# Optimization experiments

Hardware: AMD Instinct MI355X
Metric: run time of the kernel (lower is better)

## Reference

```python
import jax, jax.numpy as jnp
import numpy as np

B, S, E = 4, 2048, 768
H = 12
D = E // H  # 64

def setup_inputs() -> dict:
    key = jax.random.key(0)
    k_x, k_wqkv, k_wproj = jax.random.split(key, 3)
    x = jax.random.normal(k_x, (B, S, E), dtype=jnp.float32)
    w_qkv = jax.random.normal(k_wqkv, (E, 3 * E), dtype=jnp.float32) * 0.02
    b_qkv = jnp.zeros((3 * E,), dtype=jnp.float32)
    w_proj = jax.random.normal(k_wproj, (E, E), dtype=jnp.float32) * 0.02
    b_proj = jnp.zeros((E,), dtype=jnp.float32)
    return {"x": x, "w_qkv": w_qkv, "b_qkv": b_qkv, "w_proj": w_proj, "b_proj": b_proj}

def reference(x, w_qkv, b_qkv, w_proj, b_proj):
    # fused QKV projection: [B,S,E] -> [B,S,3E]
    qkv = jnp.einsum("bse,ef->bsf", x, w_qkv) + b_qkv
    qkv = qkv.reshape(B, S, 3, H, D)
    q, k, v = qkv[:, :, 0], qkv[:, :, 1], qkv[:, :, 2]  # [B,S,H,D]
    scale = 1.0 / jnp.sqrt(jnp.asarray(D, dtype=x.dtype))
    # causal scaled dot-product attention (explicit score matrix, as in module)
    scores = jnp.einsum("bshd,bthd->bhst", q, k) * scale  # [B,H,S,S]
    causal = jnp.tril(jnp.ones((S, S), dtype=bool))
    scores = jnp.where(causal, scores, jnp.finfo(scores.dtype).min)
    probs = jax.nn.softmax(scores, axis=-1)
    attn = jnp.einsum("bhst,bthd->bshd", probs, v).reshape(B, S, E)
    # output projection
    out = jnp.einsum("bse,ef->bsf", attn, w_proj) + b_proj
    return out
```

## Files before the change

### kernel.cpp

```cpp
#include <hip/hip_runtime.h>

#define SDIM 2048
#define EDIM 768
#define HDIM 12
#define DDIM 64
#define BDIM 4
#define MROWS (BDIM * SDIM)
#define NQKV (3 * EDIM)
#define NBH (BDIM * HDIM)
#define NTILE 32
#define NPAIR 16
#define NKT 24

typedef __attribute__((ext_vector_type(8))) short s16x8;
typedef __attribute__((ext_vector_type(4))) float f32x4;
typedef __attribute__((ext_vector_type(2))) unsigned int u32x2;

__device__ __forceinline__ short f2b(float x) {
  union { float f; unsigned u; } v; v.f = x;
  unsigned r = v.u + 0x7fffu + ((v.u >> 16) & 1u);
  return (short)(r >> 16);
}

__device__ __forceinline__ unsigned cvtpk(float lo, float hi) {
  unsigned r;
  asm volatile("v_cvt_pk_bf16_f32 %0, %1, %2" : "=v"(r) : "v"(lo), "v"(hi));
  return r;
}

__device__ __forceinline__ float fexp2(float x) {
  float r;
  asm("v_exp_f32 %0, %1" : "=v"(r) : "v"(x));
  return r;
}

__device__ __forceinline__ void gld16(const void* g, void* l) {
  __builtin_amdgcn_global_load_lds(
      (const __attribute__((address_space(1))) unsigned int*)g,
      (__attribute__((address_space(3))) unsigned int*)l, 16, 0, 0);
}

__global__ __launch_bounds__(256) void preproc(
    const float* __restrict__ x, const float* __restrict__ wqkv,
    const float* __restrict__ wproj, short* __restrict__ xb,
    short* __restrict__ wqkvt, short* __restrict__ wprojt) {
  const int bid = blockIdx.x;
  const int tid = threadIdx.x;
  const int l = tid & 63, w = tid >> 6;
  const int lr = l & 15, g = l >> 4;
  if (bid < 3072) {
    const int T = bid * 4 + w;
    const int rt = T / NKT, kt = T % NKT;
    const float* src = x + (size_t)(rt * 16 + lr) * EDIM + kt * 32 + g * 8;
    float4 v0 = *(const float4*)(src);
    float4 v1 = *(const float4*)(src + 4);
    s16x8 o;
    o[0] = f2b(v0.x); o[1] = f2b(v0.y); o[2] = f2b(v0.z); o[3] = f2b(v0.w);
    o[4] = f2b(v1.x); o[5] = f2b(v1.y); o[6] = f2b(v1.z); o[7] = f2b(v1.w);
    *(s16x8*)(xb + (size_t)T * 512 + l * 8) = o;
    return;
  }
  if (bid < 3072 + 864) {
    const int T = (bid - 3072) * 4 + w;
    const int ct = T / NKT, kt = T % NKT;
    s16x8 o;
#pragma unroll
    for (int j = 0; j < 8; ++j)
      o[j] = f2b(wqkv[(size_t)(kt * 32 + g * 8 + j) * NQKV + ct * 16 + lr]);
    *(s16x8*)(wqkvt + (size_t)T * 512 + l * 8) = o;
    return;
  }
  const int t = bid - 3072 - 864;
  const int n0 = (t % 24) * 32, k0 = (t / 24) * 32;
  __shared__ float tb[32][33];
  int tx = tid & 31, ty = tid >> 5;
#pragma unroll
  for (int i = 0; i < 4; ++i)
    tb[ty + 8 * i][tx] = wproj[(size_t)(k0 + ty + 8 * i) * EDIM + n0 + tx];
  __syncthreads();
#pragma unroll
  for (int i = 0; i < 4; ++i)
    wprojt[(size_t)(n0 + ty + 8 * i) * EDIM + k0 + tx] = f2b(tb[tx][ty + 8 * i]);
}

__global__ __launch_bounds__(256) void gemm_qkv(
    const short* __restrict__ A, const short* __restrict__ Bt,
    const float* __restrict__ bias, short* __restrict__ qout,
    short* __restrict__ kout, short* __restrict__ vout) {
  const int tid = threadIdx.x;
  const int l = tid & 63, w = tid >> 6;
  const int lr = l & 15, g = l >> 4;

  const int chunk = gridDim.x >> 3;
  const int sid = (blockIdx.x & 7) * chunk + (blockIdx.x >> 3);
  const int ntx = NQKV >> 7;
  const int bm = (sid / ntx) * 128, bn = (sid % ntx) * 128;
  const int wm = w >> 1, wn = w & 1;

  const short* Ab = A + ((size_t)(bm >> 4) + wm * 4) * NKT * 512 + l * 8;
  const short* Bb = Bt + ((size_t)(bn >> 4) + wn * 4) * NKT * 512 + l * 8;

  f32x4 acc[4][4];
  const f32x4 z4 = {0.f, 0.f, 0.f, 0.f};
#pragma unroll
  for (int m = 0; m < 4; ++m)
#pragma unroll
    for (int n = 0; n < 4; ++n) acc[m][n] = z4;

#pragma unroll 4
  for (int kt = 0; kt < NKT; ++kt) {
    s16x8 af[4], bf[4];
#pragma unroll
    for (int m = 0; m < 4; ++m)
      af[m] = *(const s16x8*)(Ab + (size_t)m * NKT * 512 + kt * 512);
#pragma unroll
    for (int n = 0; n < 4; ++n)
      bf[n] = *(const s16x8*)(Bb + (size_t)n * NKT * 512 + kt * 512);
    __builtin_amdgcn_s_setprio(1);
#pragma unroll
    for (int m = 0; m < 4; ++m)
#pragma unroll
      for (int n = 0; n < 4; ++n)
        acc[m][n] = __builtin_amdgcn_mfma_f32_16x16x32_bf16(af[m], bf[n],
                                                            acc[m][n], 0, 0, 0);
    __builtin_amdgcn_s_setprio(0);
  }

#pragma unroll
  for (int m = 0; m < 4; ++m) {
    int rbase = bm + wm * 64 + m * 16 + g * 4;
#pragma unroll
    for (int n = 0; n < 4; ++n) {
      int col = bn + wn * 64 + n * 16 + lr;
      float bv = bias[col];
      int which = (col >= 1536) ? 2 : (col >= 768 ? 1 : 0);
      int rem = col - which * 768;
      int h = rem >> 6, d = rem & 63;
#pragma unroll
      for (int i = 0; i < 4; ++i) {
        int r = rbase + i;
        int bb = r >> 11, s = r & 2047;
        short o = f2b(acc[m][n][i] + bv);
        size_t bh = (size_t)bb * HDIM + h;
        if (which == 0)      qout[(bh * SDIM + s) * DDIM + d] = o;
        else if (which == 1) kout[(bh * SDIM + s) * DDIM + d] = o;
        else                 vout[(bh * DDIM + d) * SDIM + s] = o;
      }
    }
  }
}

__global__ __launch_bounds__(256) void gemm_proj(
    const short* __restrict__ A, const short* __restrict__ Bt,
    const float* __restrict__ bias, int M, int N, int K,
    float* __restrict__ fout) {
  __shared__ char lds[3][16384];
  const int tid = threadIdx.x;
  const int l = tid & 63, w = tid >> 6;
  const int lr = l & 15, g = l >> 4;

  const int chunk = gridDim.x >> 3;
  const int sid = (blockIdx.x & 7) * chunk + (blockIdx.x >> 3);
  const int ntx = N >> 7;
  const int bm = (sid / ntx) * 128, bn = (sid % ntx) * 128;
  const int wm = w >> 1, wn = w & 1;

  const int srow = w * 32 + (l >> 2);
  const int sc8 = (((l & 3) ^ ((l >> 3) & 3)) << 3);
  const short* Ap0 = A + (size_t)(bm + srow) * K + sc8;
  const short* Bp0 = Bt + (size_t)(bn + srow) * K + sc8;

  f32x4 acc[4][4];
  const f32x4 z4 = {0.f, 0.f, 0.f, 0.f};
#pragma unroll
  for (int m = 0; m < 4; ++m)
#pragma unroll
    for (int n = 0; n < 4; ++n) acc[m][n] = z4;

#define STAGE(dst, t)                          \
  {                                            \
    char* Ad = (dst) + w * 2048;               \
    const short* Ap = Ap0 + (t) * 32;          \
    const short* Bp = Bp0 + (t) * 32;          \
    gld16(Ap, Ad);                             \
    gld16(Ap + 16 * K, Ad + 1024);             \
    gld16(Bp, Ad + 8192);                      \
    gld16(Bp + 16 * K, Ad + 9216);             \
  }

  const int nt = K >> 5;
  STAGE(lds[0], 0);
  STAGE(lds[1], 1);
  asm volatile("s_waitcnt vmcnt(4)" ::: "memory");
  __builtin_amdgcn_s_barrier();

  const int swz = ((lr >> 1) & 3) << 4;
  int bc = 0;
  for (int t = 0; t < nt; ++t) {
    if (t + 2 < nt) {
      int bs = bc + 2; if (bs >= 3) bs -= 3;
      STAGE(lds[bs], t + 2);
    }
    const char* Ab = lds[bc];
    const char* Bb = lds[bc] + 8192;
    s16x8 af[4], bfr[4];
#pragma unroll
    for (int m = 0; m < 4; ++m)
      af[m] = *(const s16x8*)(Ab + (wm * 64 + m * 16 + lr) * 64 + ((g << 4) ^ swz));
#pragma unroll
    for (int n = 0; n < 4; ++n)
      bfr[n] = *(const s16x8*)(Bb + (wn * 64 + n * 16 + lr) * 64 + ((g << 4) ^ swz));
    __builtin_amdgcn_s_setprio(1);
#pragma unroll
    for (int m = 0; m < 4; ++m)
#pragma unroll
      for (int n = 0; n < 4; ++n)
        acc[m][n] = __builtin_amdgcn_mfma_f32_16x16x32_bf16(af[m], bfr[n],
                                                            acc[m][n], 0, 0, 0);
    __builtin_amdgcn_s_setprio(0);
    if (t + 2 < nt) {
      asm volatile("s_waitcnt vmcnt(4)" ::: "memory");
      __builtin_amdgcn_s_barrier();
    } else if (t + 1 < nt) {
      asm volatile("s_waitcnt vmcnt(0)" ::: "memory");
      __builtin_amdgcn_s_barrier();
    }
    if (++bc == 3) bc = 0;
  }
#undef STAGE

#pragma unroll
  for (int m = 0; m < 4; ++m) {
    int rbase = bm + wm * 64 + m * 16 + g * 4;
#pragma unroll
    for (int n = 0; n < 4; ++n) {
      int col = bn + wn * 64 + n * 16 + lr;
      float bv = bias[col];
#pragma unroll
      for (int i = 0; i < 4; ++i)
        fout[(size_t)(rbase + i) * N + col] = acc[m][n][i] + bv;
    }
  }
}

__global__ __launch_bounds__(256, 3) void attn_mfma4(
    const short* __restrict__ qb, const short* __restrict__ kb,
    const short* __restrict__ vb, short* __restrict__ ao) {
  __shared__ short kvbuf[2][8192];
  __shared__ short pstrip[4][1024];

  const int tid = threadIdx.x;
  const int l = tid & 63, w = tid >> 6;
  const int lr = l & 15, g = l >> 4;
  const int swz = (lr & 7) << 4;

  const int lin = blockIdx.x;
  const int xcd = lin & 7;
  const int idx = lin >> 3;
  const int bh = xcd * 6 + (idx >> 4);
  const int pair = idx & 15;
  const int tiles[2] = {NTILE - 1 - pair, pair};

  const int b = bh / HDIM, h = bh % HDIM;
  const size_t base = (size_t)bh * SDIM * DDIM;

  const int srow = w * 16 + (l >> 3);
  const int sc = (l & 7) ^ (srow & 7);
  const size_t koff0 = (size_t)srow * DDIM + sc * 8;
  const size_t koff1 = (size_t)(srow + 8) * DDIM + sc * 8;
  const size_t voff0 = (size_t)srow * SDIM + sc * 8;
  const size_t voff1 = (size_t)(srow + 8) * SDIM + sc * 8;

  const float SC = 0.125f * 1.4426950408889634f;
  char* sw = (char*)pstrip[w];

#define KVSTAGE(buf_, kt_)                                        \
  {                                                               \
    char* kd = (char*)kvbuf[buf_] + w * 2048;                     \
    const short* kp = kb + base + (size_t)(kt_) * 64 * DDIM;      \
    const short* vp = vb + base + (size_t)(kt_) * 64;             \
    gld16(kp + koff0, kd);                                        \
    gld16(kp + koff1, kd + 1024);                                 \
    gld16(vp + voff0, kd + 8192);                                 \
    gld16(vp + voff1, kd + 9216);                                 \
  }

  for (int half = 0; half < 2; ++half) {
    const int tile = tiles[half];
    const int q0w = tile * 64 + w * 16;

    s16x8 qa[2];
#pragma unroll
    for (int s = 0; s < 2; ++s)
      qa[s] = *(const s16x8*)(qb + base + (size_t)(q0w + lr) * DDIM + s * 32 + g * 8);

    const f32x4 z4 = {0.f, 0.f, 0.f, 0.f};
    f32x4 acco[4];
#pragma unroll
    for (int nd = 0; nd < 4; ++nd) acco[nd] = z4;
    float mrun = -1e30f, lsum = 0.f;

    KVSTAGE(0, 0);
    {
      const int t1 = (tile >= 1) ? 1 : 0;
      KVSTAGE(1, t1);
    }

    for (int kt = 0; kt <= tile; ++kt) {
      if (kt < tile) asm volatile("s_waitcnt vmcnt(4)" ::: "memory");
      else           asm volatile("s_waitcnt vmcnt(0)" ::: "memory");
      __builtin_amdgcn_s_barrier();

      const char* Kb = (const char*)kvbuf[kt & 1];
      const char* Vb = Kb + 8192;

      f32x4 sacc[4];
#pragma unroll
      for (int nt = 0; nt < 4; ++nt) sacc[nt] = z4;
      __builtin_amdgcn_s_setprio(1);
#pragma unroll
      for (int s = 0; s < 2; ++s)
#pragma unroll
        for (int nt = 0; nt < 4; ++nt) {
          s16x8 kf = *(const s16x8*)(Kb + nt * 2048 + lr * 128 +
                                     ((s * 64 + g * 16) ^ swz));
          sacc[nt] = __builtin_amdgcn_mfma_f32_16x16x32_bf16(kf, qa[s],
                                                             sacc[nt], 0, 0, 0);
        }
      __builtin_amdgcn_s_setprio(0);

      if (kt == tile) {
        const int rloc = w * 16 + lr;
#pragma unroll
        for (int nt = 0; nt < 4; ++nt)
#pragma unroll
          for (int i = 0; i < 4; ++i)
            if (nt * 16 + g * 4 + i > rloc) sacc[nt][i] = -1e30f;
      }

      float t0 = fmaxf(fmaxf(sacc[0][0], sacc[0][1]), fmaxf(sacc[0][2], sacc[0][3]));
      float t1 = fmaxf(fmaxf(sacc[1][0], sacc[1][1]), fmaxf(sacc[1][2], sacc[1][3]));
      float t2 = fmaxf(fmaxf(sacc[2][0], sacc[2][1]), fmaxf(sacc[2][2], sacc[2][3]));
      float t3 = fmaxf(fmaxf(sacc[3][0], sacc[3][1]), fmaxf(sacc[3][2], sacc[3][3]));
      float pmax = fmaxf(fmaxf(t0, t1), fmaxf(t2, t3));
      pmax = fmaxf(pmax, __shfl_xor(pmax, 16, 64));
      pmax = fmaxf(pmax, __shfl_xor(pmax, 32, 64));

      if (__any(pmax > mrun + 44.0f)) {
        float nm = fmaxf(mrun, pmax);
        float al = fexp2((mrun - nm) * SC);
        lsum *= al;
#pragma unroll
        for (int nd = 0; nd < 4; ++nd)
#pragma unroll
          for (int i = 0; i < 4; ++i) acco[nd][i] *= al;
        mrun = nm;
      }

      const float msc = mrun * SC;
#pragma unroll
      for (int nt = 0; nt < 4; ++nt) {
        float p0 = fexp2(__builtin_fmaf(sacc[nt][0], SC, -msc));
        float p1 = fexp2(__builtin_fmaf(sacc[nt][1], SC, -msc));
        float p2 = fexp2(__builtin_fmaf(sacc[nt][2], SC, -msc));
        float p3 = fexp2(__builtin_fmaf(sacc[nt][3], SC, -msc));
        lsum += (p0 + p1) + (p2 + p3);
        u32x2 pk = {cvtpk(p0, p1), cvtpk(p2, p3)};
        *(u32x2*)(sw + lr * 128 + (((nt * 32 + g * 8) ^ swz))) = pk;
      }

      __builtin_amdgcn_s_setprio(1);
#pragma unroll
      for (int s = 0; s < 2; ++s) {
        s16x8 pf = *(const s16x8*)(sw + lr * 128 + ((s * 64 + g * 16) ^ swz));
#pragma unroll
        for (int nd = 0; nd < 4; ++nd) {
          s16x8 vf = *(const s16x8*)(Vb + nd * 2048 + lr * 128 +
                                     ((s * 64 + g * 16) ^ swz));
          acco[nd] = __builtin_amdgcn_mfma_f32_16x16x32_bf16(vf, pf,
                                                             acco[nd], 0, 0, 0);
        }
      }
      __builtin_amdgcn_s_setprio(0);

      __builtin_amdgcn_s_barrier();
      if (kt + 2 <= tile) KVSTAGE(kt & 1, kt + 2);
    }

    lsum += __shfl_xor(lsum, 16, 64);
    lsum += __shfl_xor(lsum, 32, 64);
    float inv = 1.0f / lsum;
    size_t orow = ((size_t)b * SDIM + q0w + lr) * EDIM + h * DDIM;
#pragma unroll
    for (int nd = 0; nd < 4; ++nd) {
      unsigned lo = cvtpk(acco[nd][0] * inv, acco[nd][1] * inv);
      unsigned hi = cvtpk(acco[nd][2] * inv, acco[nd][3] * inv);
      *(unsigned*)(ao + orow + nd * 16 + g * 4) = lo;
      *(unsigned*)(ao + orow + nd * 16 + g * 4 + 2) = hi;
    }
  }
#undef KVSTAGE
}

extern "C" void kernel_launch(void* const* d_in, const int* in_sizes, int n_in,
                              void* d_out, int out_size, void* d_ws,
                              size_t ws_size, hipStream_t stream) {
  const float* x = (const float*)d_in[0];
  const float* w_qkv = (const float*)d_in[1];
  const float* b_qkv = (const float*)d_in[2];
  const float* w_proj = (const float*)d_in[3];
  const float* b_proj = (const float*)d_in[4];
  float* out = (float*)d_out;

  char* p = (char*)d_ws;
  short* xb = (short*)p;      p += (size_t)MROWS * EDIM * 2;
  short* wqkvt = (short*)p;   p += (size_t)NQKV * EDIM * 2;
  short* wprojt = (short*)p;  p += (size_t)EDIM * EDIM * 2;
  short* qbuf = (short*)p;    p += (size_t)NBH * SDIM * DDIM * 2;
  short* kbuf = (short*)p;    p += (size_t)NBH * SDIM * DDIM * 2;
  short* vbuf = (short*)p;    p += (size_t)NBH * SDIM * DDIM * 2;
  short* aob = (short*)p;     p += (size_t)MROWS * EDIM * 2;

  dim3 blk(256);
  preproc<<<dim3(3072 + 864 + 576), blk, 0, stream>>>(x, w_qkv, w_proj, xb,
                                                      wqkvt, wprojt);
  gemm_qkv<<<dim3((MROWS / 128) * (NQKV / 128)), blk, 0, stream>>>(
      xb, wqkvt, b_qkv, qbuf, kbuf, vbuf);
  attn_mfma4<<<dim3(NPAIR * NBH), blk, 0, stream>>>(qbuf, kbuf, vbuf, aob);
  gemm_proj<<<dim3((MROWS / 128) * (EDIM / 128)), blk, 0, stream>>>(
      aob, wprojt, b_proj, MROWS, EDIM, EDIM, out);
}
```

Measured before the change: 145.4 us.

## Stage QKV weights through swizzled LDS with 128x256 tiles and triple buffering

```diff
diff --git a/kernel.cpp b/kernel.cpp
--- a/kernel.cpp
+++ b/kernel.cpp
@@ -46,9 +46,9 @@
     short* __restrict__ wqkvt, short* __restrict__ wprojt) {
   const int bid = blockIdx.x;
   const int tid = threadIdx.x;
-  const int l = tid & 63, w = tid >> 6;
-  const int lr = l & 15, g = l >> 4;
   if (bid < 3072) {
+    const int l = tid & 63, w = tid >> 6;
+    const int lr = l & 15, g = l >> 4;
     const int T = bid * 4 + w;
     const int rt = T / NKT, kt = T % NKT;
     const float* src = x + (size_t)(rt * 16 + lr) * EDIM + kt * 32 + g * 8;
@@ -60,78 +60,116 @@
     *(s16x8*)(xb + (size_t)T * 512 + l * 8) = o;
     return;
   }
-  if (bid < 3072 + 864) {
-    const int T = (bid - 3072) * 4 + w;
-    const int ct = T / NKT, kt = T % NKT;
-    s16x8 o;
-#pragma unroll
-    for (int j = 0; j < 8; ++j)
-      o[j] = f2b(wqkv[(size_t)(kt * 32 + g * 8 + j) * NQKV + ct * 16 + lr]);
-    *(s16x8*)(wqkvt + (size_t)T * 512 + l * 8) = o;
-    return;
-  }
-  const int t = bid - 3072 - 864;
-  const int n0 = (t % 24) * 32, k0 = (t / 24) * 32;
+  const float* in; short* out; int N, t;
+  if (bid < 4800) { t = bid - 3072; in = wqkv; out = wqkvt; N = NQKV; }
+  else { t = bid - 4800; in = wproj; out = wprojt; N = EDIM; }
+  const int ntx = N / 32;
+  int n0 = (t % ntx) * 32, k0 = (t / ntx) * 32;
   __shared__ float tb[32][33];
   int tx = tid & 31, ty = tid >> 5;
 #pragma unroll
   for (int i = 0; i < 4; ++i)
-    tb[ty + 8 * i][tx] = wproj[(size_t)(k0 + ty + 8 * i) * EDIM + n0 + tx];
+    tb[ty + 8 * i][tx] = in[(size_t)(k0 + ty + 8 * i) * N + n0 + tx];
   __syncthreads();
 #pragma unroll
   for (int i = 0; i < 4; ++i)
-    wprojt[(size_t)(n0 + ty + 8 * i) * EDIM + k0 + tx] = f2b(tb[tx][ty + 8 * i]);
+    out[(size_t)(n0 + ty + 8 * i) * EDIM + k0 + tx] = f2b(tb[tx][ty + 8 * i]);
 }
 
 __global__ __launch_bounds__(256) void gemm_qkv(
     const short* __restrict__ A, const short* __restrict__ Bt,
     const float* __restrict__ bias, short* __restrict__ qout,
     short* __restrict__ kout, short* __restrict__ vout) {
+  __shared__ char lds[3][16384];
   const int tid = threadIdx.x;
   const int l = tid & 63, w = tid >> 6;
   const int lr = l & 15, g = l >> 4;
+  const int K = EDIM;
 
   const int chunk = gridDim.x >> 3;
   const int sid = (blockIdx.x & 7) * chunk + (blockIdx.x >> 3);
-  const int ntx = NQKV >> 7;
-  const int bm = (sid / ntx) * 128, bn = (sid % ntx) * 128;
+  const int ntx = NQKV >> 8;
+  const int bm = (sid / ntx) << 7;
+  const int bn = (sid % ntx) << 8;
   const int wm = w >> 1, wn = w & 1;
 
-  const short* Ab = A + ((size_t)(bm >> 4) + wm * 4) * NKT * 512 + l * 8;
-  const short* Bb = Bt + ((size_t)(bn >> 4) + wn * 4) * NKT * 512 + l * 8;
-
-  f32x4 acc[4][4];
+  const int sck = (((tid & 3) ^ ((tid >> 3) & 3)) << 3);
+  const short* Bp0 = Bt + (size_t)(bn + w * 64 + ((tid & 63) >> 2)) * K + sck;
+
+  const short* Abase = A + ((size_t)(bm >> 4) + wm * 4) * NKT * 512 + l * 8;
+
+  f32x4 acc[4][8];
   const f32x4 z4 = {0.f, 0.f, 0.f, 0.f};
 #pragma unroll
-  for (int m = 0; m < 4; ++m)
-#pragma unroll
-    for (int n = 0; n < 4; ++n) acc[m][n] = z4;
-
-#pragma unroll 4
-  for (int kt = 0; kt < NKT; ++kt) {
-    s16x8 af[4], bf[4];
-#pragma unroll
-    for (int m = 0; m < 4; ++m)
-      af[m] = *(const s16x8*)(Ab + (size_t)m * NKT * 512 + kt * 512);
-#pragma unroll
-    for (int n = 0; n < 4; ++n)
-      bf[n] = *(const s16x8*)(Bb + (size_t)n * NKT * 512 + kt * 512);
+  for (int mf = 0; mf < 4; ++mf)
+#pragma unroll
+    for (int nf = 0; nf < 8; ++nf) acc[mf][nf] = z4;
+
+#define STAGEB(s_, t_)                                   \
+  {                                                      \
+    char* d_ = lds[s_] + w * 4096;                       \
+    const short* p_ = Bp0 + (t_) * 32;                   \
+    gld16(p_, d_);                                       \
+    gld16(p_ + 16 * K, d_ + 1024);                       \
+    gld16(p_ + 32 * K, d_ + 2048);                       \
+    gld16(p_ + 48 * K, d_ + 3072);                       \
+  }
+#define LOADA(dst_, t_)                                          \
+  {                                                              \
+    _Pragma("unroll")                                            \
+    for (int mf = 0; mf < 4; ++mf)                               \
+      dst_[mf] = *(const s16x8*)(Abase + (size_t)mf * NKT * 512 + (t_) * 512); \
+  }
+
+  s16x8 afc[4], afn[4], bf[8];
+
+  STAGEB(0, 0);
+  STAGEB(1, 1);
+  LOADA(afc, 0);
+  asm volatile("s_waitcnt vmcnt(8)" ::: "memory");
+  __builtin_amdgcn_s_barrier();
+
+  const int rsw = ((lr >> 1) & 3) << 4;
+  for (int t = 0; t < NKT; ++t) {
+    if (t + 1 < NKT) LOADA(afn, t + 1);
+    if (t + 2 < NKT) {
+      int bs = t + 2; while (bs >= 3) bs -= 3;
+      STAGEB(bs, t + 2);
+    }
+    const char* Bb = lds[t % 3];
+    s16x8 a0 = afc[0], a1 = afc[1], a2 = afc[2], a3 = afc[3];
+#pragma unroll
+    for (int nf = 0; nf < 8; ++nf)
+      bf[nf] = *(const s16x8*)(Bb + (wn * 128 + nf * 16 + lr) * 64 +
+                               ((g << 4) ^ rsw));
     __builtin_amdgcn_s_setprio(1);
 #pragma unroll
-    for (int m = 0; m < 4; ++m)
-#pragma unroll
-      for (int n = 0; n < 4; ++n)
-        acc[m][n] = __builtin_amdgcn_mfma_f32_16x16x32_bf16(af[m], bf[n],
-                                                            acc[m][n], 0, 0, 0);
+    for (int nf = 0; nf < 8; ++nf) {
+      acc[0][nf] = __builtin_amdgcn_mfma_f32_16x16x32_bf16(a0, bf[nf], acc[0][nf], 0, 0, 0);
+      acc[1][nf] = __builtin_amdgcn_mfma_f32_16x16x32_bf16(a1, bf[nf], acc[1][nf], 0, 0, 0);
+      acc[2][nf] = __builtin_amdgcn_mfma_f32_16x16x32_bf16(a2, bf[nf], acc[2][nf], 0, 0, 0);
+      acc[3][nf] = __builtin_amdgcn_mfma_f32_16x16x32_bf16(a3, bf[nf], acc[3][nf], 0, 0, 0);
+    }
     __builtin_amdgcn_s_setprio(0);
-  }
-
-#pragma unroll
-  for (int m = 0; m < 4; ++m) {
-    int rbase = bm + wm * 64 + m * 16 + g * 4;
-#pragma unroll
-    for (int n = 0; n < 4; ++n) {
-      int col = bn + wn * 64 + n * 16 + lr;
+#pragma unroll
+    for (int mf = 0; mf < 4; ++mf) afc[mf] = afn[mf];
+    if (t + 2 < NKT) {
+      asm volatile("s_waitcnt vmcnt(8)" ::: "memory");
+      __builtin_amdgcn_s_barrier();
+    } else if (t + 1 < NKT) {
+      asm volatile("s_waitcnt vmcnt(4)" ::: "memory");
+      __builtin_amdgcn_s_barrier();
+    }
+  }
+#undef STAGEB
+#undef LOADA
+
+#pragma unroll
+  for (int mf = 0; mf < 4; ++mf) {
+    int rbase = bm + wm * 64 + mf * 16 + g * 4;
+#pragma unroll
+    for (int nf = 0; nf < 8; ++nf) {
+      int col = bn + wn * 128 + nf * 16 + lr;
       float bv = bias[col];
       int which = (col >= 1536) ? 2 : (col >= 768 ? 1 : 0);
       int rem = col - which * 768;
@@ -140,7 +178,7 @@
       for (int i = 0; i < 4; ++i) {
         int r = rbase + i;
         int bb = r >> 11, s = r & 2047;
-        short o = f2b(acc[m][n][i] + bv);
+        short o = f2b(acc[mf][nf][i] + bv);
         size_t bh = (size_t)bb * HDIM + h;
         if (which == 0)      qout[(bh * SDIM + s) * DDIM + d] = o;
         else if (which == 1) kout[(bh * SDIM + s) * DDIM + d] = o;
@@ -422,10 +460,9 @@
   short* aob = (short*)p;     p += (size_t)MROWS * EDIM * 2;
 
   dim3 blk(256);
-  preproc<<<dim3(3072 + 864 + 576), blk, 0, stream>>>(x, w_qkv, w_proj, xb,
-                                                      wqkvt, wprojt);
-  gemm_qkv<<<dim3((MROWS / 128) * (NQKV / 128)), blk, 0, stream>>>(
-      xb, wqkvt, b_qkv, qbuf, kbuf, vbuf);
+  preproc<<<dim3(3072 + 1728 + 576), blk, 0, stream>>>(x, w_qkv, w_proj, xb,
+                                                       wqkvt, wprojt);
+  gemm_qkv<<<dim3(576), blk, 0, stream>>>(xb, wqkvt, b_qkv, qbuf, kbuf, vbuf);
   attn_mfma4<<<dim3(NPAIR * NBH), blk, 0, stream>>>(qbuf, kbuf, vbuf, aob);
   gemm_proj<<<dim3((MROWS / 128) * (EDIM / 128)), blk, 0, stream>>>(
       aob, wprojt, b_proj, MROWS, EDIM, EDIM, out);
```

After: 181.3 us. +24.7%, slower.
